# Kernel tuning notes

Hardware: AMD Instinct MI355X
Metric: run time of the kernel (lower is better)

Reference implementation:

```python
import jax, jax.numpy as jnp
import numpy as np

N_NODES = 100000

def setup_inputs() -> dict:
    key = jax.random.key(0)
    k1, k2 = jax.random.split(key)
    x = jax.random.normal(k1, (N_NODES, 48), dtype=jnp.float32)
    edge_index = jax.random.randint(k2, (2, 1600000), 0, N_NODES, dtype=jnp.int64)
    return {"x": x, "edge_index": edge_index}

def reference(x, edge_index):
    # adj = SparseTensor.from_edge_index(edge_index): row=edge_index[0], col=edge_index[1]
    # adj.matmul(x): out[i] = sum over edges with row==i of x[col]
    row, col = edge_index[0], edge_index[1]
    x_neighbors_sum = jax.ops.segment_sum(x[col], row, num_segments=x.shape[0])  # [N, D]
    node_labels = jnp.concatenate((x, x_neighbors_sum), axis=-1)  # [N, 2D]
    return node_labels
```

## Files before the change

kernel.cpp:

```cpp
#include <hip/hip_runtime.h>


constexpr int D_IN  = 48;
constexpr int BSH   = 7;
constexpr int BNODES = 1 << BSH;
constexpr int MAXNB = 1024;
constexpr int CAPB  = 2400;
constexpr int OVF_MAX = 4096;

constexpr int PT_THREADS = 256;
constexpr int PT_ITEMS   = 16;
constexpr int PT_TILE    = PT_THREADS * PT_ITEMS;

constexpr int AG_THREADS = 512;
constexpr int AG_ITEMS   = 5;


__device__ __forceinline__ unsigned int bf16rne(float f) {
    unsigned int u = __float_as_uint(f);
    return (u + 0x7fffu + ((u >> 16) & 1u)) >> 16;
}
__device__ __forceinline__ unsigned int packbf(float a, float b) {
    return bf16rne(a) | (bf16rne(b) << 16);
}
__device__ __forceinline__ void accbf(float4& a, uint2 u) {
    a.x += __uint_as_float(u.x << 16);
    a.y += __uint_as_float(u.x & 0xffff0000u);
    a.z += __uint_as_float(u.y << 16);
    a.w += __uint_as_float(u.y & 0xffff0000u);
}
__device__ __forceinline__ void add4(float4& a, const float4& b) {
    a.x += b.x; a.y += b.y; a.z += b.z; a.w += b.w;
}


__global__ void convert_copy_kernel(const float4* __restrict__ x4,
                                    uint4* __restrict__ x2u4,
                                    float4* __restrict__ out4, int n_nodes) {
    int i = blockIdx.x * blockDim.x + threadIdx.x;
    if (i >= n_nodes * 6) return;
    int n = i / 6, s = i - n * 6;
    float4 v0 = x4[(size_t)n * 12 + 2 * s];
    float4 v1 = x4[(size_t)n * 12 + 2 * s + 1];
    out4[(size_t)n * 24 + 2 * s]     = v0;
    out4[(size_t)n * 24 + 2 * s + 1] = v1;
    x2u4[(size_t)n * 6 + s] = make_uint4(packbf(v0.x, v0.y), packbf(v0.z, v0.w),
                                         packbf(v1.x, v1.y), packbf(v1.z, v1.w));
}


__global__ __launch_bounds__(PT_THREADS)
void partition_kernel(const int* __restrict__ row, const int* __restrict__ col,
                      int* __restrict__ gcursor, unsigned int* __restrict__ pairs,
                      int* __restrict__ ovf_cnt, uint2* __restrict__ ovf,
                      int n_edges, int nb) {
    __shared__ int hist[MAXNB];
    __shared__ int offs[MAXNB];
    __shared__ int gbase[MAXNB];
    __shared__ int scanbuf[PT_THREADS];

    int t = threadIdx.x;
    int tile0 = blockIdx.x * PT_TILE;

    for (int i = t; i < nb; i += PT_THREADS) hist[i] = 0;
    __syncthreads();

    int r[PT_ITEMS], c[PT_ITEMS];
#pragma unroll
    for (int j = 0; j < PT_ITEMS; ++j) {
        int e = tile0 + j * PT_THREADS + t;
        if (e < n_edges) {
            r[j] = row[e];
            c[j] = col[e];
            atomicAdd(&hist[r[j] >> BSH], 1);
        } else {
            r[j] = -1;
        }
    }
    __syncthreads();

    int cb = t * 4;
    int loc[4];
    int s = 0;
#pragma unroll
    for (int j = 0; j < 4; ++j) {
        int i = cb + j;
        loc[j] = (i < nb) ? hist[i] : 0;
        s += loc[j];
    }
    scanbuf[t] = s;
    __syncthreads();
    for (int off = 1; off < PT_THREADS; off <<= 1) {
        int v = (t >= off) ? scanbuf[t - off] : 0;
        __syncthreads();
        scanbuf[t] += v;
        __syncthreads();
    }
    int run = (t == 0) ? 0 : scanbuf[t - 1];
#pragma unroll
    for (int j = 0; j < 4; ++j) {
        int i = cb + j;
        if (i < nb) { offs[i] = run; run += loc[j]; }
    }
    __syncthreads();

    for (int i = t; i < nb; i += PT_THREADS) {
        int cnt = hist[i];
        gbase[i] = cnt ? (atomicAdd(&gcursor[i], cnt) - offs[i]) : 0;
        hist[i] = offs[i];
    }
    __syncthreads();

#pragma unroll
    for (int j = 0; j < PT_ITEMS; ++j) {
        if (r[j] >= 0) {
            int b = r[j] >> BSH;
            int lpos = atomicAdd(&hist[b], 1);
            int g = gbase[b] + lpos;
            if (g < CAPB) {
                pairs[(size_t)b * CAPB + g] =
                    ((unsigned int)(r[j] & (BNODES - 1)) << 17) | (unsigned int)c[j];
            } else {
                int o = atomicAdd(ovf_cnt, 1);
                if (o < OVF_MAX)
                    ovf[o] = make_uint2((unsigned int)r[j], (unsigned int)c[j]);
            }
        }
    }
}


template <int USE_BF16>
__global__ __launch_bounds__(AG_THREADS)
void agg_kernel(const float4* __restrict__ x4, const uint2* __restrict__ xbv,
                const unsigned int* __restrict__ pairs,
                const int* __restrict__ gcursor,
                float4* __restrict__ out4, int n_nodes) {
    __shared__ unsigned int scol[CAPB];
    __shared__ int hist[BNODES];
    __shared__ int offs[BNODES];
    __shared__ int cur[BNODES];
    __shared__ int hs[BNODES];

    int t   = threadIdx.x;
    int bkt = blockIdx.x;
    int cnt = min(gcursor[bkt], CAPB);
    const unsigned int* pb = pairs + (size_t)bkt * CAPB;

    if (t < BNODES) hist[t] = 0;
    __syncthreads();

    unsigned int pv[AG_ITEMS];
#pragma unroll
    for (int j = 0; j < AG_ITEMS; ++j) {
        int idx = t + j * AG_THREADS;
        if (idx < cnt) {
            pv[j] = pb[idx];
            atomicAdd(&hist[pv[j] >> 17], 1);
        }
    }
    __syncthreads();

    if (t < BNODES) hs[t] = hist[t];
    __syncthreads();
    for (int off = 1; off < BNODES; off <<= 1) {
        int v = (t >= off && t < BNODES) ? hs[t - off] : 0;
        __syncthreads();
        if (t < BNODES) hs[t] += v;
        __syncthreads();
    }
    if (t < BNODES) {
        offs[t] = hs[t] - hist[t];
        cur[t]  = offs[t];
    }
    __syncthreads();

#pragma unroll
    for (int j = 0; j < AG_ITEMS; ++j) {
        int idx = t + j * AG_THREADS;
        if (idx < cnt) {
            int pos = atomicAdd(&cur[pv[j] >> 17], 1);
            scol[pos] = pv[j] & 0x1FFFFu;
        }
    }
    __syncthreads();

    int n  = t >> 2;
    int qt = t & 3;
    float4 a0 = make_float4(0.f, 0.f, 0.f, 0.f);
    float4 a1 = make_float4(0.f, 0.f, 0.f, 0.f);
    float4 a2 = make_float4(0.f, 0.f, 0.f, 0.f);

    int k0 = offs[n];
    int k1 = k0 + hist[n];
    int k  = k0;
    if constexpr (USE_BF16) {
        for (; k + 2 <= k1; k += 2) {
            const uint2* p0 = xbv + (size_t)scol[k]     * 12 + qt * 3;
            const uint2* p1 = xbv + (size_t)scol[k + 1] * 12 + qt * 3;
            uint2 u0 = p0[0], u1 = p0[1], u2 = p0[2];
            uint2 w0 = p1[0], w1 = p1[1], w2 = p1[2];
            accbf(a0, u0); accbf(a1, u1); accbf(a2, u2);
            accbf(a0, w0); accbf(a1, w1); accbf(a2, w2);
        }
        if (k < k1) {
            const uint2* p0 = xbv + (size_t)scol[k] * 12 + qt * 3;
            accbf(a0, p0[0]); accbf(a1, p0[1]); accbf(a2, p0[2]);
        }
    } else {
        for (; k + 2 <= k1; k += 2) {
            size_t c0 = (size_t)scol[k]     * 12 + qt * 3;
            size_t c1 = (size_t)scol[k + 1] * 12 + qt * 3;
            float4 u0 = x4[c0], u1 = x4[c0 + 1], u2 = x4[c0 + 2];
            float4 w0 = x4[c1], w1 = x4[c1 + 1], w2 = x4[c1 + 2];
            add4(a0, u0); add4(a1, u1); add4(a2, u2);
            add4(a0, w0); add4(a1, w1); add4(a2, w2);
        }
        if (k < k1) {
            size_t c0 = (size_t)scol[k] * 12 + qt * 3;
            add4(a0, x4[c0]); add4(a1, x4[c0 + 1]); add4(a2, x4[c0 + 2]);
        }
    }

    int node = (bkt << BSH) + n;
    if (node < n_nodes) {
        size_t ob = (size_t)node * 24;
        out4[ob + 12 + qt * 3 + 0] = a0;
        out4[ob + 12 + qt * 3 + 1] = a1;
        out4[ob + 12 + qt * 3 + 2] = a2;
        if constexpr (!USE_BF16) {
            size_t xb = (size_t)node * 12;
            out4[ob + qt * 3 + 0] = x4[xb + qt * 3 + 0];
            out4[ob + qt * 3 + 1] = x4[xb + qt * 3 + 1];
            out4[ob + qt * 3 + 2] = x4[xb + qt * 3 + 2];
        }
    }
}


__global__ void ovf_kernel(const float* __restrict__ x, const uint2* __restrict__ ovf,
                           const int* __restrict__ ovf_cnt, float* __restrict__ out) {
    int cnt = min(*ovf_cnt, OVF_MAX);
    int total = cnt * D_IN;
    for (int idx = blockIdx.x * blockDim.x + threadIdx.x; idx < total;
         idx += gridDim.x * blockDim.x) {
        int e = idx / D_IN, d = idx - e * D_IN;
        uint2 rc = ovf[e];
        atomicAdd(&out[(size_t)rc.x * 96 + 48 + d], x[(size_t)rc.y * 48 + d]);
    }
}


__global__ void init_out_kernel(const float4* __restrict__ x4,
                                float4* __restrict__ out4, int n_nodes) {
    int idx = blockIdx.x * blockDim.x + threadIdx.x;
    int total = n_nodes * 24;
    if (idx >= total) return;
    int i = idx / 24;
    int q = idx - i * 24;
    out4[idx] = (q < 12) ? x4[i * 12 + q] : make_float4(0.f, 0.f, 0.f, 0.f);
}

__global__ void scatter_add_kernel(const float* __restrict__ x,
                                   const int* __restrict__ row,
                                   const int* __restrict__ col,
                                   float* __restrict__ out, int n_edges) {
    long long gid = (long long)blockIdx.x * blockDim.x + threadIdx.x;
    long long total = (long long)n_edges * D_IN;
    if (gid >= total) return;
    int e = (int)(gid / D_IN);
    int d = (int)(gid - (long long)e * D_IN);
    atomicAdd(out + (long long)row[e] * 96 + D_IN + d,
              x[(long long)col[e] * D_IN + d]);
}


extern "C" void kernel_launch(void* const* d_in, const int* in_sizes, int n_in,
                              void* d_out, int out_size, void* d_ws, size_t ws_size,
                              hipStream_t stream) {
    const float* x  = (const float*)d_in[0];
    const int*   ei = (const int*)d_in[1];
    float*       out = (float*)d_out;

    int n_nodes = in_sizes[0] / D_IN;
    int n_edges = in_sizes[1] / 2;
    const int* row = ei;
    const int* col = ei + n_edges;

    int nb = (n_nodes + BNODES - 1) >> BSH;
    int ntiles = (n_edges + PT_TILE - 1) / PT_TILE;
    bool col_fits = n_nodes <= (1 << 17);

    size_t t2_bytes = ((size_t)nb * CAPB + nb + 1 + 2 * (size_t)OVF_MAX) * 4;
    size_t x2_off   = (t2_bytes + 15) & ~(size_t)15;
    size_t t1_bytes = x2_off + (size_t)n_nodes * 96;

    if (nb > MAXNB || !col_fits || ws_size < t2_bytes) {
        int init_total = n_nodes * 24;
        init_out_kernel<<<(init_total + 255) / 256, 256, 0, stream>>>(
            (const float4*)x, (float4*)out, n_nodes);
        long long total = (long long)n_edges * D_IN;
        scatter_add_kernel<<<(int)((total + 255) / 256), 256, 0, stream>>>(
            x, row, col, out, n_edges);
        return;
    }

    unsigned int* pairs = (unsigned int*)d_ws;
    int* gcursor = (int*)(pairs + (size_t)nb * CAPB);
    int* ovf_cnt = gcursor + nb;
    uint2* ovf   = (uint2*)(ovf_cnt + 1);
    bool bf16_tier = (ws_size >= t1_bytes);
    uint4* x2u4  = (uint4*)((char*)d_ws + x2_off);

    hipMemsetAsync(gcursor, 0, (size_t)(nb + 1) * sizeof(int), stream);

    if (bf16_tier) {
        int ct = n_nodes * 6;
        convert_copy_kernel<<<(ct + 255) / 256, 256, 0, stream>>>(
            (const float4*)x, x2u4, (float4*)out, n_nodes);
    }

    partition_kernel<<<ntiles, PT_THREADS, 0, stream>>>(
        row, col, gcursor, pairs, ovf_cnt, ovf, n_edges, nb);

    if (bf16_tier) {
        agg_kernel<1><<<nb, AG_THREADS, 0, stream>>>(
            (const float4*)x, (const uint2*)x2u4, pairs, gcursor,
            (float4*)out, n_nodes);
    } else {
        agg_kernel<0><<<nb, AG_THREADS, 0, stream>>>(
            (const float4*)x, nullptr, pairs, gcursor,
            (float4*)out, n_nodes);
    }

    ovf_kernel<<<16, 256, 0, stream>>>(x, ovf, ovf_cnt, out);
}
```

Measured before the change: 88.00 us.

## Fuse bf16 conversion into partition kernel, fold overflow into aggregation, unroll gather

Merges the x-to-bf16 conversion and output copy into the partition launch as extra blocks, so both run concurrently in one launch. It also removes the separate overflow kernel by having each aggregation thread scan the overflow list and add matching edges in registers, and it unrolls the bf16 gather loop from 2 to 4 neighbours. The goal is fewer kernel launches and more memory-level parallelism in the gather. The cost is that every aggregation thread now loops over the overflow count, which becomes expensive if overflow is large.

```diff
diff --git a/kernel.cpp b/kernel.cpp
--- a/kernel.cpp
+++ b/kernel.cpp
@@ -34,32 +34,35 @@
 }
 
 
-__global__ void convert_copy_kernel(const float4* __restrict__ x4,
-                                    uint4* __restrict__ x2u4,
-                                    float4* __restrict__ out4, int n_nodes) {
-    int i = blockIdx.x * blockDim.x + threadIdx.x;
-    if (i >= n_nodes * 6) return;
-    int n = i / 6, s = i - n * 6;
-    float4 v0 = x4[(size_t)n * 12 + 2 * s];
-    float4 v1 = x4[(size_t)n * 12 + 2 * s + 1];
-    out4[(size_t)n * 24 + 2 * s]     = v0;
-    out4[(size_t)n * 24 + 2 * s + 1] = v1;
-    x2u4[(size_t)n * 6 + s] = make_uint4(packbf(v0.x, v0.y), packbf(v0.z, v0.w),
-                                         packbf(v1.x, v1.y), packbf(v1.z, v1.w));
-}
-
-
 __global__ __launch_bounds__(PT_THREADS)
-void partition_kernel(const int* __restrict__ row, const int* __restrict__ col,
-                      int* __restrict__ gcursor, unsigned int* __restrict__ pairs,
-                      int* __restrict__ ovf_cnt, uint2* __restrict__ ovf,
-                      int n_edges, int nb) {
+void prep_kernel(const int* __restrict__ row, const int* __restrict__ col,
+                 int* __restrict__ gcursor, unsigned int* __restrict__ pairs,
+                 int* __restrict__ ovf_cnt, uint2* __restrict__ ovf,
+                 const float4* __restrict__ x4, uint4* __restrict__ x2u4,
+                 float4* __restrict__ out4,
+                 int n_edges, int nb, int ntiles, int n_nodes) {
     __shared__ int hist[MAXNB];
     __shared__ int offs[MAXNB];
     __shared__ int gbase[MAXNB];
     __shared__ int scanbuf[PT_THREADS];
 
     int t = threadIdx.x;
+
+    if (blockIdx.x >= ntiles) {
+        int i = (blockIdx.x - ntiles) * PT_THREADS + t;
+        if (i < n_nodes * 6) {
+            int n = i / 6, s = i - n * 6;
+            float4 v0 = x4[(size_t)n * 12 + 2 * s];
+            float4 v1 = x4[(size_t)n * 12 + 2 * s + 1];
+            out4[(size_t)n * 24 + 2 * s]     = v0;
+            out4[(size_t)n * 24 + 2 * s + 1] = v1;
+            x2u4[(size_t)n * 6 + s] =
+                make_uint4(packbf(v0.x, v0.y), packbf(v0.z, v0.w),
+                           packbf(v1.x, v1.y), packbf(v1.z, v1.w));
+        }
+        return;
+    }
+
     int tile0 = blockIdx.x * PT_TILE;
 
     for (int i = t; i < nb; i += PT_THREADS) hist[i] = 0;
@@ -135,6 +138,7 @@
 void agg_kernel(const float4* __restrict__ x4, const uint2* __restrict__ xbv,
                 const unsigned int* __restrict__ pairs,
                 const int* __restrict__ gcursor,
+                const int* __restrict__ ovf_cnt, const uint2* __restrict__ ovf,
                 float4* __restrict__ out4, int n_nodes) {
     __shared__ unsigned int scol[CAPB];
     __shared__ int hist[BNODES];
@@ -195,15 +199,21 @@
     int k1 = k0 + hist[n];
     int k  = k0;
     if constexpr (USE_BF16) {
-        for (; k + 2 <= k1; k += 2) {
-            const uint2* p0 = xbv + (size_t)scol[k]     * 12 + qt * 3;
-            const uint2* p1 = xbv + (size_t)scol[k + 1] * 12 + qt * 3;
-            uint2 u0 = p0[0], u1 = p0[1], u2 = p0[2];
-            uint2 w0 = p1[0], w1 = p1[1], w2 = p1[2];
-            accbf(a0, u0); accbf(a1, u1); accbf(a2, u2);
-            accbf(a0, w0); accbf(a1, w1); accbf(a2, w2);
-        }
-        if (k < k1) {
+        for (; k + 4 <= k1; k += 4) {
+            const uint2* pA = xbv + (size_t)scol[k]     * 12 + qt * 3;
+            const uint2* pB = xbv + (size_t)scol[k + 1] * 12 + qt * 3;
+            const uint2* pC = xbv + (size_t)scol[k + 2] * 12 + qt * 3;
+            const uint2* pD = xbv + (size_t)scol[k + 3] * 12 + qt * 3;
+            uint2 A0 = pA[0], A1 = pA[1], A2 = pA[2];
+            uint2 B0 = pB[0], B1 = pB[1], B2 = pB[2];
+            uint2 C0 = pC[0], C1 = pC[1], C2 = pC[2];
+            uint2 D0 = pD[0], D1 = pD[1], D2 = pD[2];
+            accbf(a0, A0); accbf(a1, A1); accbf(a2, A2);
+            accbf(a0, B0); accbf(a1, B1); accbf(a2, B2);
+            accbf(a0, C0); accbf(a1, C1); accbf(a2, C2);
+            accbf(a0, D0); accbf(a1, D1); accbf(a2, D2);
+        }
+        for (; k < k1; ++k) {
             const uint2* p0 = xbv + (size_t)scol[k] * 12 + qt * 3;
             accbf(a0, p0[0]); accbf(a1, p0[1]); accbf(a2, p0[2]);
         }
@@ -219,6 +229,15 @@
         if (k < k1) {
             size_t c0 = (size_t)scol[k] * 12 + qt * 3;
             add4(a0, x4[c0]); add4(a1, x4[c0 + 1]); add4(a2, x4[c0 + 2]);
+        }
+    }
+
+    int oc = min(*ovf_cnt, OVF_MAX);
+    for (int i = 0; i < oc; ++i) {
+        uint2 rc = ovf[i];
+        if ((int)(rc.x >> BSH) == bkt && (int)(rc.x & (BNODES - 1)) == n) {
+            const float4* xr = x4 + (size_t)rc.y * 12 + qt * 3;
+            add4(a0, xr[0]); add4(a1, xr[1]); add4(a2, xr[2]);
         }
     }
 
@@ -238,19 +257,6 @@
 }
 
 
-__global__ void ovf_kernel(const float* __restrict__ x, const uint2* __restrict__ ovf,
-                           const int* __restrict__ ovf_cnt, float* __restrict__ out) {
-    int cnt = min(*ovf_cnt, OVF_MAX);
-    int total = cnt * D_IN;
-    for (int idx = blockIdx.x * blockDim.x + threadIdx.x; idx < total;
-         idx += gridDim.x * blockDim.x) {
-        int e = idx / D_IN, d = idx - e * D_IN;
-        uint2 rc = ovf[e];
-        atomicAdd(&out[(size_t)rc.x * 96 + 48 + d], x[(size_t)rc.y * 48 + d]);
-    }
-}
-
-
 __global__ void init_out_kernel(const float4* __restrict__ x4,
                                 float4* __restrict__ out4, int n_nodes) {
     int idx = blockIdx.x * blockDim.x + threadIdx.x;
@@ -314,24 +320,18 @@
 
     hipMemsetAsync(gcursor, 0, (size_t)(nb + 1) * sizeof(int), stream);
 
-    if (bf16_tier) {
-        int ct = n_nodes * 6;
-        convert_copy_kernel<<<(ct + 255) / 256, 256, 0, stream>>>(
-            (const float4*)x, x2u4, (float4*)out, n_nodes);
-    }
-
-    partition_kernel<<<ntiles, PT_THREADS, 0, stream>>>(
-        row, col, gcursor, pairs, ovf_cnt, ovf, n_edges, nb);
+    int conv_blocks = bf16_tier ? (n_nodes * 6 + PT_THREADS - 1) / PT_THREADS : 0;
+    prep_kernel<<<ntiles + conv_blocks, PT_THREADS, 0, stream>>>(
+        row, col, gcursor, pairs, ovf_cnt, ovf,
+        (const float4*)x, x2u4, (float4*)out, n_edges, nb, ntiles, n_nodes);
 
     if (bf16_tier) {
         agg_kernel<1><<<nb, AG_THREADS, 0, stream>>>(
             (const float4*)x, (const uint2*)x2u4, pairs, gcursor,
-            (float4*)out, n_nodes);
+            ovf_cnt, ovf, (float4*)out, n_nodes);
     } else {
         agg_kernel<0><<<nb, AG_THREADS, 0, stream>>>(
             (const float4*)x, nullptr, pairs, gcursor,
-            (float4*)out, n_nodes);
-    }
-
-    ovf_kernel<<<16, 256, 0, stream>>>(x, ovf, ovf_cnt, out);
-}
+            ovf_cnt, ovf, (float4*)out, n_nodes);
+    }
+}
```

After: 85.32 us. 3.0% less time.
